# Kernel tuning notes

Measured on AMD Instinct MI355X. Metric: run time of the kernel, lower is better.

## Reference

```python
import jax, jax.numpy as jnp
import numpy as np

B, N, C, H = 8, 1024, 1024, 16
D = C // H
SCALE = D ** -0.5


def setup_inputs() -> dict:
    key = jax.random.key(0)
    ks = jax.random.split(key, 5)
    s = 0.02  # keep pre-softmax logits in a sane range
    return {
        "x": jax.random.normal(ks[0], (B, N, C), dtype=jnp.float32),
        "Wq": jax.random.normal(ks[1], (C, C), dtype=jnp.float32) * s,
        "bq": jax.random.normal(ks[2], (C,), dtype=jnp.float32) * s,
        "Wkv": jax.random.normal(ks[3], (C, 2 * C), dtype=jnp.float32) * s,
        "bkv": jax.random.normal(ks[4], (2 * C,), dtype=jnp.float32) * s,
    }


def reference(x, Wq, bq, Wkv, bkv):
    b, n, c = x.shape
    h, d = H, c // H
    q = (x @ Wq + bq).reshape(b, n, h, d)                 # [b,n,h,d]
    kv = x @ Wkv + bkv                                     # [b,n,2c]
    k, v = jnp.split(kv, 2, axis=-1)                       # each [b,n,c]
    k = k.reshape(b, n, h, d)
    v = v.reshape(b, n, h, d)
    att = jnp.einsum("bnhd,bmhd->bnmh", q, k) * SCALE      # [b,n,m,h]
    att = jax.nn.softmax(att, axis=2)                      # softmax over keys (m)
    out = jnp.einsum("bnmh,bmhd->bnhd", att, v).reshape(b, n, c)
    return out
```

## Files before the change

kernel.cpp:

```cpp
#include <hip/hip_runtime.h>
#include <stdint.h>

using u16 = unsigned short;
using u32 = unsigned int;
using bf16x8 = __attribute__((ext_vector_type(8))) __bf16;
using f32x4  = __attribute__((ext_vector_type(4))) float;

#define NB 8
#define NN 1024
#define NC 1024
#define NH 16
#define ND 64
#define QSCALE 0.18033688011112042f

__device__ __forceinline__ u16 f2bf(float f) {
  u32 u = __float_as_uint(f);
  return (u16)((u + 0x7fffu + ((u >> 16) & 1u)) >> 16);
}
__device__ __forceinline__ u16 bfc(float f) {
  __bf16 b = (__bf16)f;
  return __builtin_bit_cast(u16, b);
}
__device__ __forceinline__ u32 pack2(u16 a, u16 b) { return (u32)a | ((u32)b << 16); }

__device__ __forceinline__ void gload16(const void* g, void* l) {
  __builtin_amdgcn_global_load_lds((__attribute__((address_space(1))) const u32*)g,
                                   (__attribute__((address_space(3))) u32*)l, 16, 0, 0);
}

__global__ void k_prep(const float* __restrict__ x, const float* __restrict__ Wq,
                       const float* __restrict__ bq, const float* __restrict__ Wkv,
                       const float* __restrict__ bkv,
                       u16* __restrict__ xb, u16* __restrict__ Wt, float* __restrict__ bias) {
  __shared__ u16 tile[64][72];
  int bid = blockIdx.x;
  int t = threadIdx.x;
  if (bid < 8192) {
    int i = bid * 256 + t;
    float4 v = ((const float4*)x)[i];
    ((uint2*)xb)[i] = make_uint2(pack2(f2bf(v.x), f2bf(v.y)), pack2(f2bf(v.z), f2bf(v.w)));
    return;
  }
  if (bid < 8960) {
    int pb = bid - 8192;
    int k0 = (pb & 15) << 6;
    int c0 = (pb >> 4) << 6;
    bool isQ = (c0 < 1024);
    const float* src = isQ ? Wq : Wkv;
    int ldw  = isQ ? 1024 : 2048;
    int csrc = isQ ? c0 : (c0 - 1024);
    float sc = isQ ? QSCALE : 1.0f;

    int r  = t >> 2;
    int cq = (t & 3) << 4;
    const float* p = src + (size_t)(k0 + r) * ldw + csrc + cq;
#pragma unroll
    for (int j = 0; j < 16; j += 4) {
      float4 v = *(const float4*)(p + j);
      tile[r][cq + j + 0] = f2bf(v.x * sc);
      tile[r][cq + j + 1] = f2bf(v.y * sc);
      tile[r][cq + j + 2] = f2bf(v.z * sc);
      tile[r][cq + j + 3] = f2bf(v.w * sc);
    }
    __syncthreads();
    int co = t >> 2;
    int kq = (t & 3) << 4;
    u16 v0[16];
#pragma unroll
    for (int j = 0; j < 16; ++j) v0[j] = tile[kq + j][co];
    uint4 o0, o1;
    o0.x = pack2(v0[0], v0[1]);  o0.y = pack2(v0[2], v0[3]);
    o0.z = pack2(v0[4], v0[5]);  o0.w = pack2(v0[6], v0[7]);
    o1.x = pack2(v0[8], v0[9]);  o1.y = pack2(v0[10], v0[11]);
    o1.z = pack2(v0[12], v0[13]); o1.w = pack2(v0[14], v0[15]);
    u16* dst = Wt + (size_t)(c0 + co) * 1024 + k0 + kq;
    *(uint4*)dst = o0;
    *(uint4*)(dst + 8) = o1;
    return;
  }
  {
    int i = (bid - 8960) * 256 + t;
    if (i < 1024) bias[i] = bq[i] * QSCALE;
    else if (i < 3072) bias[i] = bkv[i - 1024];
  }
}

__launch_bounds__(512, 2)
__global__ void k_gemm(const u16* __restrict__ A, const u16* __restrict__ Bw,
                       const float* __restrict__ bias,
                       u16* __restrict__ qws, u16* __restrict__ kws, u16* __restrict__ vtw) {
  __shared__ __align__(16) u16 LA[2][16384];
  __shared__ __align__(16) u16 LB[2][12288];
  int flat = blockIdx.x;
  int swz = (flat & 7) * 64 + (flat >> 3);
  int m0 = (swz & 31) * 256;
  int n0 = (swz >> 5) * 192;
  int tid = threadIdx.x;
  int w = tid >> 6, lane = tid & 63;
  int lo = lane & 15, hi = lane >> 4;
  int wm = w >> 2, wn = w & 3;

  f32x4 acc[8][3] = {};

  int cs = ((tid & 7) ^ ((tid >> 3) & 7)) * 8;
  const u16* Ag = A  + (size_t)(m0 + (tid >> 3)) * 1024 + cs;
  const u16* Bg = Bw + (size_t)(n0 + (tid >> 3)) * 1024 + cs;

  int ck0 = ((hi ^ (lo & 7)) << 3);
  int ck1 = (((4 + hi) ^ (lo & 7)) << 3);
  const u16* laR = &LA[0][wm * 8192 + lo * 64];
  const u16* lbR = &LB[0][(wn * 48 + lo) * 64];

#define MFMA_(a, b, c) __builtin_amdgcn_mfma_f32_16x16x32_bf16(a, b, c, 0, 0, 0)
#define SBAR() __builtin_amdgcn_sched_barrier(0); __builtin_amdgcn_s_barrier(); __builtin_amdgcn_sched_barrier(0)
#define LGKM0() asm volatile("s_waitcnt lgkmcnt(0)" ::: "memory"); __builtin_amdgcn_sched_barrier(0)

#define ST_AH(BUF, MH, KT)                                                                     \
  gload16(Ag + (size_t)((MH) * 128) * 1024 + (KT) * 64,      &LA[BUF][(MH) * 8192 + tid * 8]); \
  gload16(Ag + (size_t)((MH) * 128 + 64) * 1024 + (KT) * 64, &LA[BUF][(MH) * 8192 + 4096 + tid * 8]);
#define ST_BT(BUF, NH, KT)                                                                     \
  gload16(Bg + (size_t)((NH) * 64) * 1024 + (KT) * 64,       &LB[BUF][(NH) * 4096 + tid * 8]);

#define QUAD(Q, NI)                                                           \
  __builtin_amdgcn_s_setprio(1);                                              \
  _Pragma("unroll")                                                           \
  for (int ks = 0; ks < 2; ++ks)                                              \
    _Pragma("unroll")                                                         \
    for (int mi = 0; mi < 4; ++mi)                                            \
      acc[(Q) * 4 + mi][NI] = MFMA_(af[mi][ks], bfr[NI][ks], acc[(Q) * 4 + mi][NI]); \
  __builtin_amdgcn_s_setprio(0);

  ST_AH(0, 0, 0); ST_AH(0, 1, 0); ST_BT(0, 0, 0); ST_BT(0, 1, 0); ST_BT(0, 2, 0);
  ST_AH(1, 0, 1); ST_AH(1, 1, 1); ST_BT(1, 0, 1); ST_BT(1, 1, 1); ST_BT(1, 2, 1);
  asm volatile("s_waitcnt vmcnt(7)" ::: "memory");
  __builtin_amdgcn_s_barrier();

#pragma unroll 1
  for (int t = 0; t < 16; ++t) {
    int b = t & 1;
    const u16* la = laR + b * 16384;
    const u16* lb = lbR + b * 12288;
    bf16x8 af[4][2], bfr[3][2];
    bool st = (t < 14);

#pragma unroll
    for (int mi = 0; mi < 4; ++mi) {
      af[mi][0] = *(const bf16x8*)(la + mi * 1024 + ck0);
      af[mi][1] = *(const bf16x8*)(la + mi * 1024 + ck1);
    }
    bfr[0][0] = *(const bf16x8*)(lb + ck0);
    bfr[0][1] = *(const bf16x8*)(lb + ck1);
    SBAR();
    LGKM0();
    QUAD(0, 0);
    SBAR();

    bfr[1][0] = *(const bf16x8*)(lb + 1024 + ck0);
    bfr[1][1] = *(const bf16x8*)(lb + 1024 + ck1);
    SBAR();
    LGKM0();
    QUAD(0, 1);
    SBAR();

    bfr[2][0] = *(const bf16x8*)(lb + 2048 + ck0);
    bfr[2][1] = *(const bf16x8*)(lb + 2048 + ck1);
    SBAR();
    LGKM0();
    QUAD(0, 2);
    SBAR();

#pragma unroll
    for (int mi = 0; mi < 4; ++mi) {
      af[mi][0] = *(const bf16x8*)(la + (4 + mi) * 1024 + ck0);
      af[mi][1] = *(const bf16x8*)(la + (4 + mi) * 1024 + ck1);
    }
    if (st) { ST_BT(b, 0, t + 2); }
    SBAR();
    LGKM0();
    QUAD(1, 0);
    SBAR();

    if (st) { ST_AH(b, 0, t + 2); ST_BT(b, 1, t + 2); }
    SBAR();
    QUAD(1, 1);
    SBAR();

    if (st) { ST_AH(b, 1, t + 2); ST_BT(b, 2, t + 2); }
    SBAR();
    QUAD(1, 2);
    if (t < 14)       { asm volatile("s_waitcnt vmcnt(7)" ::: "memory"); }
    else if (t == 14) { asm volatile("s_waitcnt vmcnt(0)" ::: "memory"); }
    SBAR();
  }
#undef QUAD
#undef ST_AH
#undef ST_BT
#undef SBAR
#undef LGKM0
#undef MFMA_

#pragma unroll
  for (int ni = 0; ni < 3; ++ni) {
    int c = n0 + wn * 48 + ni * 16 + lo;
    float bvl = bias[c];
    if (c < 2048) {
#pragma unroll
      for (int mi = 0; mi < 8; ++mi) {
#pragma unroll
        for (int r = 0; r < 4; ++r) {
          int m = m0 + wm * 128 + mi * 16 + hi * 4 + r;
          int b = m >> 10, tok = m & 1023;
          u16 o = f2bf(acc[mi][ni][r] + bvl);
          if (c < 1024) {
            int h = c >> 6, d = c & 63;
            qws[((size_t)(b * 16 + h) * 1024 + tok) * 64 + d] = o;
          } else {
            int c2 = c - 1024; int h = c2 >> 6, d = c2 & 63;
            kws[((size_t)(b * 16 + h) * 1024 + tok) * 64 + d] = o;
          }
        }
      }
    } else {
      int c2 = c - 2048; int h = c2 >> 6, d = c2 & 63;
#pragma unroll
      for (int mi = 0; mi < 8; ++mi) {
        int m = m0 + wm * 128 + mi * 16 + hi * 4;
        int b = m >> 10, tok = m & 1023;
        ushort4 pk;
        pk.x = bfc(acc[mi][ni][0] + bvl);
        pk.y = bfc(acc[mi][ni][1] + bvl);
        pk.z = bfc(acc[mi][ni][2] + bvl);
        pk.w = bfc(acc[mi][ni][3] + bvl);
        *(ushort4*)&vtw[((size_t)(b * 16 + h) * 64 + d) * 1024 + tok] = pk;
      }
    }
  }
}

__launch_bounds__(512)
__global__ void k_attn(const u16* __restrict__ q, const u16* __restrict__ k,
                       const u16* __restrict__ vt, float* __restrict__ out) {
  __shared__ __align__(16) u16 Ks[2][4096];
  __shared__ __align__(16) u16 Vs[2][4096];
  __shared__ __align__(16) u16 P[8][16][72];
  int bh = blockIdx.x;
  int q0 = blockIdx.y * 128;
  int tid = threadIdx.x;
  int w = tid >> 6, lane = tid & 63;
  int lo = lane & 15, hi = lane >> 4;
  int b = bh >> 4, h = bh & 15;

  const u16* kbase = k  + (size_t)bh * 65536;
  const u16* vbase = vt + (size_t)bh * 65536;

  int srow = w * 8 + (lane >> 3);
  int cg   = (lane & 7) ^ ((lane >> 3) & 7);
  const u16* gK = kbase + (size_t)srow * 64   + cg * 8;
  const u16* gV = vbase + (size_t)srow * 1024 + cg * 8;
  u16* lK0 = &Ks[0][w * 512];
  u16* lK1 = &Ks[1][w * 512];
  u16* lV0 = &Vs[0][w * 512];
  u16* lV1 = &Vs[1][w * 512];

  const u16* qp = q + ((size_t)bh * 1024 + q0 + w * 16 + lo) * 64 + hi * 8;
  bf16x8 qf0 = *(const bf16x8*)(qp);
  bf16x8 qf1 = *(const bf16x8*)(qp + 32);

  f32x4 acc_o[4] = {};
  float m_s = -1e30f;
  float l_s = 0.f;

  int sw = lo & 7;

  gload16(gK, lK0);
  gload16(gV, lV0);
  __syncthreads();

  for (int t = 0; t < 16; ++t) {
    int cur = t & 1;
    if (t < 15) {
      gload16(gK + (t + 1) * 4096, cur ? lK0 : lK1);
      gload16(gV + (t + 1) * 64,   cur ? lV0 : lV1);
    }
    f32x4 s[4] = {};
    const u16* kb = Ks[cur];
#pragma unroll
    for (int ni = 0; ni < 4; ++ni) {
      const u16* kp = kb + (ni * 16 + lo) * 64;
      bf16x8 kf0 = *(const bf16x8*)(kp + ((hi ^ sw) * 8));
      bf16x8 kf1 = *(const bf16x8*)(kp + (((4 + hi) ^ sw) * 8));
      s[ni] = __builtin_amdgcn_mfma_f32_16x16x32_bf16(kf0, qf0, s[ni], 0, 0, 0);
      s[ni] = __builtin_amdgcn_mfma_f32_16x16x32_bf16(kf1, qf1, s[ni], 0, 0, 0);
    }
    float pm;
    {
      float a0 = fmaxf(fmaxf(s[0][0], s[0][1]), fmaxf(s[0][2], s[0][3]));
      float a1 = fmaxf(fmaxf(s[1][0], s[1][1]), fmaxf(s[1][2], s[1][3]));
      float a2 = fmaxf(fmaxf(s[2][0], s[2][1]), fmaxf(s[2][2], s[2][3]));
      float a3 = fmaxf(fmaxf(s[3][0], s[3][1]), fmaxf(s[3][2], s[3][3]));
      pm = fmaxf(fmaxf(a0, a1), fmaxf(a2, a3));
      pm = fmaxf(pm, __shfl_xor(pm, 16));
      pm = fmaxf(pm, __shfl_xor(pm, 32));
    }
    if (!__all(pm <= m_s + 8.0f)) {
      float mn = fmaxf(m_s, pm);
      float corr = __builtin_amdgcn_exp2f(m_s - mn);
      m_s = mn;
      l_s *= corr;
      float cr[4];
#pragma unroll
      for (int r = 0; r < 4; ++r) cr[r] = __shfl(corr, hi * 4 + r);
#pragma unroll
      for (int ci = 0; ci < 4; ++ci)
#pragma unroll
        for (int r = 0; r < 4; ++r) acc_o[ci][r] *= cr[r];
    }
    float rs = 0.f;
#pragma unroll
    for (int ni = 0; ni < 4; ++ni) {
      float p0 = __builtin_amdgcn_exp2f(s[ni][0] - m_s);
      float p1 = __builtin_amdgcn_exp2f(s[ni][1] - m_s);
      float p2 = __builtin_amdgcn_exp2f(s[ni][2] - m_s);
      float p3 = __builtin_amdgcn_exp2f(s[ni][3] - m_s);
      rs += (p0 + p1) + (p2 + p3);
      ushort4 pk;
      pk.x = bfc(p0); pk.y = bfc(p1); pk.z = bfc(p2); pk.w = bfc(p3);
      *(ushort4*)&P[w][lo][ni * 16 + hi * 4] = pk;
    }
    rs += __shfl_xor(rs, 16);
    rs += __shfl_xor(rs, 32);
    l_s += rs;
    bf16x8 pf0 = *(const bf16x8*)(&P[w][lo][hi * 8]);
    bf16x8 pf1 = *(const bf16x8*)(&P[w][lo][32 + hi * 8]);
    const u16* vb = Vs[cur];
#pragma unroll
    for (int ci = 0; ci < 4; ++ci) {
      const u16* vp = vb + (ci * 16 + lo) * 64;
      bf16x8 vf0 = *(const bf16x8*)(vp + ((hi ^ sw) * 8));
      bf16x8 vf1 = *(const bf16x8*)(vp + (((4 + hi) ^ sw) * 8));
      acc_o[ci] = __builtin_amdgcn_mfma_f32_16x16x32_bf16(pf0, vf0, acc_o[ci], 0, 0, 0);
      acc_o[ci] = __builtin_amdgcn_mfma_f32_16x16x32_bf16(pf1, vf1, acc_o[ci], 0, 0, 0);
    }
    __syncthreads();
  }
  float inv = 1.0f / l_s;
  float ivr[4];
#pragma unroll
  for (int r = 0; r < 4; ++r) ivr[r] = __shfl(inv, hi * 4 + r);
#pragma unroll
  for (int r = 0; r < 4; ++r) {
    int n = q0 + w * 16 + hi * 4 + r;
    float* dst = out + ((size_t)(b * 1024 + n)) * 1024 + h * 64;
#pragma unroll
    for (int ci = 0; ci < 4; ++ci) dst[ci * 16 + lo] = acc_o[ci][r] * ivr[r];
  }
}

extern "C" void kernel_launch(void* const* d_in, const int* in_sizes, int n_in,
                              void* d_out, int out_size, void* d_ws, size_t ws_size,
                              hipStream_t stream) {
  const float* x   = (const float*)d_in[0];
  const float* Wq  = (const float*)d_in[1];
  const float* bq  = (const float*)d_in[2];
  const float* Wkv = (const float*)d_in[3];
  const float* bkv = (const float*)d_in[4];
  float* out = (float*)d_out;

  char* ws = (char*)d_ws;
  u16*   xb   = (u16*)(ws);
  u16*   Wt   = (u16*)(ws + 16777216);
  float* bias = (float*)(ws + 23068672);
  u16*   qws  = (u16*)(ws + 23080960);
  u16*   kws  = (u16*)(ws + 39858176);
  u16*   vtw  = (u16*)(ws + 73412608);

  k_prep<<<8972, 256, 0, stream>>>(x, Wq, bq, Wkv, bkv, xb, Wt, bias);
  k_gemm<<<512, 512, 0, stream>>>(xb, Wt, bias, qws, kws, vtw);
  {
    dim3 g(128, 8);
    k_attn<<<g, 512, 0, stream>>>(qws, kws, vtw, out);
  }
}
```

Before: 138.9 us.

## Fold bias prep into GEMM epilogue, remap GEMM tiles per XCD, prioritize MFMA waves

Drops the bias-preparation blocks from the prep kernel and computes the scaled bias directly in the GEMM epilogue from bq/bkv, removing a small workspace buffer and some blocks. Changes the GEMM block-to-tile mapping so each XCD gets a contiguous group of M tiles, which is meant to improve L2 reuse of A rows. Wraps the attention MFMA loops with s_setprio so MFMA-issuing waves are preferred over others. These are small, independent tweaks, and the effects of the mapping and priority changes depend on how the scheduler behaves.

```diff
diff --git a/kernel.cpp b/kernel.cpp
--- a/kernel.cpp
+++ b/kernel.cpp
@@ -29,9 +29,8 @@
 }
 
 __global__ void k_prep(const float* __restrict__ x, const float* __restrict__ Wq,
-                       const float* __restrict__ bq, const float* __restrict__ Wkv,
-                       const float* __restrict__ bkv,
-                       u16* __restrict__ xb, u16* __restrict__ Wt, float* __restrict__ bias) {
+                       const float* __restrict__ Wkv,
+                       u16* __restrict__ xb, u16* __restrict__ Wt) {
   __shared__ u16 tile[64][72];
   int bid = blockIdx.x;
   int t = threadIdx.x;
@@ -41,7 +40,7 @@
     ((uint2*)xb)[i] = make_uint2(pack2(f2bf(v.x), f2bf(v.y)), pack2(f2bf(v.z), f2bf(v.w)));
     return;
   }
-  if (bid < 8960) {
+  {
     int pb = bid - 8192;
     int k0 = (pb & 15) << 6;
     int c0 = (pb >> 4) << 6;
@@ -76,25 +75,19 @@
     u16* dst = Wt + (size_t)(c0 + co) * 1024 + k0 + kq;
     *(uint4*)dst = o0;
     *(uint4*)(dst + 8) = o1;
-    return;
-  }
-  {
-    int i = (bid - 8960) * 256 + t;
-    if (i < 1024) bias[i] = bq[i] * QSCALE;
-    else if (i < 3072) bias[i] = bkv[i - 1024];
   }
 }
 
 __launch_bounds__(512, 2)
 __global__ void k_gemm(const u16* __restrict__ A, const u16* __restrict__ Bw,
-                       const float* __restrict__ bias,
+                       const float* __restrict__ bq, const float* __restrict__ bkv,
                        u16* __restrict__ qws, u16* __restrict__ kws, u16* __restrict__ vtw) {
   __shared__ __align__(16) u16 LA[2][16384];
   __shared__ __align__(16) u16 LB[2][12288];
   int flat = blockIdx.x;
-  int swz = (flat & 7) * 64 + (flat >> 3);
-  int m0 = (swz & 31) * 256;
-  int n0 = (swz >> 5) * 192;
+  int xcd = flat & 7, idx = flat >> 3;
+  int m0 = (xcd * 4 + (idx & 3)) * 256;
+  int n0 = (idx >> 2) * 192;
   int tid = threadIdx.x;
   int w = tid >> 6, lane = tid & 63;
   int lo = lane & 15, hi = lane >> 4;
@@ -202,7 +195,7 @@
 #pragma unroll
   for (int ni = 0; ni < 3; ++ni) {
     int c = n0 + wn * 48 + ni * 16 + lo;
-    float bvl = bias[c];
+    float bvl = (c < 1024) ? bq[c] * QSCALE : bkv[c - 1024];
     if (c < 2048) {
 #pragma unroll
       for (int mi = 0; mi < 8; ++mi) {
@@ -284,6 +277,7 @@
     }
     f32x4 s[4] = {};
     const u16* kb = Ks[cur];
+    __builtin_amdgcn_s_setprio(1);
 #pragma unroll
     for (int ni = 0; ni < 4; ++ni) {
       const u16* kp = kb + (ni * 16 + lo) * 64;
@@ -292,6 +286,7 @@
       s[ni] = __builtin_amdgcn_mfma_f32_16x16x32_bf16(kf0, qf0, s[ni], 0, 0, 0);
       s[ni] = __builtin_amdgcn_mfma_f32_16x16x32_bf16(kf1, qf1, s[ni], 0, 0, 0);
     }
+    __builtin_amdgcn_s_setprio(0);
     float pm;
     {
       float a0 = fmaxf(fmaxf(s[0][0], s[0][1]), fmaxf(s[0][2], s[0][3]));
@@ -333,6 +328,7 @@
     bf16x8 pf0 = *(const bf16x8*)(&P[w][lo][hi * 8]);
     bf16x8 pf1 = *(const bf16x8*)(&P[w][lo][32 + hi * 8]);
     const u16* vb = Vs[cur];
+    __builtin_amdgcn_s_setprio(1);
 #pragma unroll
     for (int ci = 0; ci < 4; ++ci) {
       const u16* vp = vb + (ci * 16 + lo) * 64;
@@ -341,6 +337,7 @@
       acc_o[ci] = __builtin_amdgcn_mfma_f32_16x16x32_bf16(pf0, vf0, acc_o[ci], 0, 0, 0);
       acc_o[ci] = __builtin_amdgcn_mfma_f32_16x16x32_bf16(pf1, vf1, acc_o[ci], 0, 0, 0);
     }
+    __builtin_amdgcn_s_setprio(0);
     __syncthreads();
   }
   float inv = 1.0f / l_s;
@@ -369,13 +366,12 @@
   char* ws = (char*)d_ws;
   u16*   xb   = (u16*)(ws);
   u16*   Wt   = (u16*)(ws + 16777216);
-  float* bias = (float*)(ws + 23068672);
   u16*   qws  = (u16*)(ws + 23080960);
   u16*   kws  = (u16*)(ws + 39858176);
   u16*   vtw  = (u16*)(ws + 73412608);
 
-  k_prep<<<8972, 256, 0, stream>>>(x, Wq, bq, Wkv, bkv, xb, Wt, bias);
-  k_gemm<<<512, 512, 0, stream>>>(xb, Wt, bias, qws, kws, vtw);
+  k_prep<<<8960, 256, 0, stream>>>(x, Wq, Wkv, xb, Wt);
+  k_gemm<<<512, 512, 0, stream>>>(xb, Wt, bq, bkv, qws, kws, vtw);
   {
     dim3 g(128, 8);
     k_attn<<<g, 512, 0, stream>>>(qws, kws, vtw, out);
```

After: 137.1 us. Within noise of the previous version (-1.2%).
